# Kernel optimization log

Hardware: AMD Instinct MI355X
Metric: run time of the kernel (lower is better)

## Reference

```python
import jax, jax.numpy as jnp
import numpy as np

EPS_RMS = 1e-6
Q_CLIP_MIN = 1e-5

def setup_inputs() -> dict:
    key = jax.random.key(0)
    k1, k2 = jax.random.split(key)
    x = jax.random.normal(k1, (1, 2048, 4096), dtype=jnp.float32)
    # kaiming_uniform-ish init for weight [in_features, out_features]
    fan_in = 4096
    bound = 1.0 / np.sqrt(fan_in)
    weight = jax.random.uniform(k2, (4096, 4096), dtype=jnp.float32, minval=-bound, maxval=bound)
    rms_weight = jnp.ones((4096,), dtype=jnp.float32)
    return {"x": x, "weight": weight, "rms_weight": rms_weight}

def reference(x, weight, rms_weight):
    # RMSNorm over last dim
    xn = x * jax.lax.rsqrt(jnp.mean(x * x, axis=-1, keepdims=True) + EPS_RMS) * rms_weight
    K = weight.shape[0]
    orig_shape = xn.shape
    x2 = xn.reshape(-1, K)  # [M, K]

    # per-tensor absmax int8 activation quantization
    a_scale = 127.0 / jnp.clip(jnp.max(jnp.abs(x2)), Q_CLIP_MIN)
    A_q = jnp.clip(jnp.round(x2 * a_scale), -128.0, 127.0)

    # absmean ternary weight quantization
    b_scale = 1.0 / jnp.clip(jnp.mean(jnp.abs(weight)), Q_CLIP_MIN)
    B_t = jnp.clip(jnp.round(weight * b_scale), -1.0, 1.0)

    # integer matmul + dequant: (A_q @ B_t) / (a_scale * b_scale)
    out = (A_q @ B_t) / (a_scale * b_scale)  # [M, N]
    return out.reshape(*orig_shape[:-1], weight.shape[1])
```

## Files before the change

### kernel.cpp

```cpp
#include <hip/hip_runtime.h>
#include <cstdint>

#define M_DIM 2048
#define K_DIM 4096
#define N_DIM 4096

#define BM 256
#define BN 128
#define BK 128
#define KT (K_DIM / BK)
#define A_TILE_BYTES (BM * BK)
#define B_TILE_BYTES (BN * BK)
#define TILE_BYTES (A_TILE_BYTES + B_TILE_BYTES)
#define NBUF 3
#define LDS_BYTES (NBUF * TILE_BYTES)

typedef __attribute__((ext_vector_type(4))) int i32x4;

__device__ __forceinline__ void gload_lds16(const void* g, void* l) {
  __builtin_amdgcn_global_load_lds(
      (__attribute__((address_space(1))) void*)(g),
      (__attribute__((address_space(3))) void*)(l), 16, 0, 0);
}

__global__ void fused_reduce_kernel(const float* __restrict__ x,
                                    const float* __restrict__ rw,
                                    const float* __restrict__ w,
                                    float* __restrict__ invrms,
                                    float* __restrict__ rowmax,
                                    double* __restrict__ partials) {
  const int tid = threadIdx.x;
  __shared__ double red[4];
  __shared__ float redf[4];
  __shared__ float sInv;

  if (blockIdx.x < 2048) {
    const int row = blockIdx.x;
    const float4* xr = (const float4*)(x + (size_t)row * K_DIM);
    const float4* wr = (const float4*)rw;
    float4 xv[4];
    double ss = 0.0;
#pragma unroll
    for (int i = 0; i < 4; i++) {
      xv[i] = xr[i * 256 + tid];
      ss += (double)xv[i].x * xv[i].x + (double)xv[i].y * xv[i].y +
            (double)xv[i].z * xv[i].z + (double)xv[i].w * xv[i].w;
    }
    for (int off = 32; off; off >>= 1) ss += __shfl_down(ss, off);
    if ((tid & 63) == 0) red[tid >> 6] = ss;
    __syncthreads();
    if (tid == 0) {
      double t = red[0] + red[1] + red[2] + red[3];
      sInv = (float)(1.0 / sqrt(t * (1.0 / (double)K_DIM) + 1e-6));
    }
    __syncthreads();
    const float inv = sInv;
    if (tid == 0) invrms[row] = inv;

    float amax = 0.f;
#pragma unroll
    for (int i = 0; i < 4; i++) {
      float4 wv = wr[i * 256 + tid];
      amax = fmaxf(amax, fabsf((xv[i].x * inv) * wv.x));
      amax = fmaxf(amax, fabsf((xv[i].y * inv) * wv.y));
      amax = fmaxf(amax, fabsf((xv[i].z * inv) * wv.z));
      amax = fmaxf(amax, fabsf((xv[i].w * inv) * wv.w));
    }
    for (int off = 32; off; off >>= 1) amax = fmaxf(amax, __shfl_down(amax, off));
    if ((tid & 63) == 0) redf[tid >> 6] = amax;
    __syncthreads();
    if (tid == 0)
      rowmax[row] = fmaxf(fmaxf(redf[0], redf[1]), fmaxf(redf[2], redf[3]));
  } else {
    const int bid = blockIdx.x - 2048;
    const float4* w4 = (const float4*)w;
    const size_t base = (size_t)bid * 2048;
    double s = 0.0;
#pragma unroll
    for (int i = 0; i < 8; i++) {
      float4 v = w4[base + i * 256 + tid];
      s += (double)((fabsf(v.x) + fabsf(v.y)) + (fabsf(v.z) + fabsf(v.w)));
    }
    for (int off = 32; off; off >>= 1) s += __shfl_down(s, off);
    if ((tid & 63) == 0) red[tid >> 6] = s;
    __syncthreads();
    if (tid == 0) partials[bid] = red[0] + red[1] + red[2] + red[3];
  }
}

__global__ void scales_kernel(const float* __restrict__ rowmax,
                              const double* __restrict__ partials,
                              float* __restrict__ scales) {
  const int tid = threadIdx.x;
  float m = 0.f;
  double s = 0.0;
#pragma unroll
  for (int i = 0; i < 8; i++) {
    m = fmaxf(m, rowmax[i * 256 + tid]);
    s += partials[i * 256 + tid];
  }
  for (int off = 32; off; off >>= 1) {
    m = fmaxf(m, __shfl_down(m, off));
    s += __shfl_down(s, off);
  }
  __shared__ float redf[4];
  __shared__ double red[4];
  if ((tid & 63) == 0) { redf[tid >> 6] = m; red[tid >> 6] = s; }
  __syncthreads();
  if (tid == 0) {
    float amax = fmaxf(fmaxf(redf[0], redf[1]), fmaxf(redf[2], redf[3]));
    double wsum = red[0] + red[1] + red[2] + red[3];
    float as = 127.0f / fmaxf(amax, 1e-5f);
    float mean_f = (float)(wsum * (1.0 / 16777216.0));
    float bs = 1.0f / fmaxf(mean_f, 1e-5f);
    scales[0] = as;
    scales[1] = bs;
    scales[2] = 1.0f / (as * bs);
  }
}

__global__ void fused_quant_kernel(const float* __restrict__ x,
                                   const float* __restrict__ rw,
                                   const float* __restrict__ invrms,
                                   const float* __restrict__ scales,
                                   const float* __restrict__ w,
                                   char* __restrict__ Aq,
                                   char* __restrict__ Bt) {
  const int tid = threadIdx.x;
  if (blockIdx.x < 2048) {
    const int row = blockIdx.x;
    const float inv = invrms[row];
    const float as = scales[0];
    const float4* xr = (const float4*)(x + (size_t)row * K_DIM);
    const float4* wr = (const float4*)rw;
    union { char c[16]; int4 v; } o;
#pragma unroll
    for (int i = 0; i < 4; i++) {
      float4 xv = xr[tid * 4 + i];
      float4 wv = wr[tid * 4 + i];
      float t0 = (xv.x * inv) * wv.x;
      float t1 = (xv.y * inv) * wv.y;
      float t2 = (xv.z * inv) * wv.z;
      float t3 = (xv.w * inv) * wv.w;
      o.c[i * 4 + 0] = (char)(int)fminf(fmaxf(rintf(t0 * as), -128.f), 127.f);
      o.c[i * 4 + 1] = (char)(int)fminf(fmaxf(rintf(t1 * as), -128.f), 127.f);
      o.c[i * 4 + 2] = (char)(int)fminf(fmaxf(rintf(t2 * as), -128.f), 127.f);
      o.c[i * 4 + 3] = (char)(int)fminf(fmaxf(rintf(t3 * as), -128.f), 127.f);
    }
    *(int4*)(Aq + (size_t)row * K_DIM + tid * 16) = o.v;
  } else {
    __shared__ float lds[64][68];
    const int tile = blockIdx.x - 2048;
    const int n0 = (tile & 63) * 64;
    const int k0 = (tile >> 6) * 64;
    const float bs = scales[1];
#pragma unroll
    for (int i = 0; i < 4; i++) {
      const int id = i * 256 + tid;
      const int r = id >> 4;
      const int c4 = (id & 15) * 4;
      float4 v = *(const float4*)(w + (size_t)(k0 + r) * N_DIM + n0 + c4);
      lds[c4 + 0][r] = fminf(fmaxf(rintf(v.x * bs), -1.f), 1.f);
      lds[c4 + 1][r] = fminf(fmaxf(rintf(v.y * bs), -1.f), 1.f);
      lds[c4 + 2][r] = fminf(fmaxf(rintf(v.z * bs), -1.f), 1.f);
      lds[c4 + 3][r] = fminf(fmaxf(rintf(v.w * bs), -1.f), 1.f);
    }
    __syncthreads();
    const int rn = tid >> 2;
    const int kg = (tid & 3) * 16;
    union { char c[16]; int4 v; } o;
#pragma unroll
    for (int j = 0; j < 16; j++) o.c[j] = (char)(int)lds[rn][kg + j];
    *(int4*)(Bt + (size_t)(n0 + rn) * K_DIM + k0 + kg) = o.v;
  }
}

__global__ void __launch_bounds__(256, 1)
gemm_kernel(const char* __restrict__ Aq, const char* __restrict__ Bt,
            float* __restrict__ out, const float* __restrict__ scales) {
  extern __shared__ char lds[];
  const int tid = threadIdx.x;
  const int lane = tid & 63;
  const int wave = tid >> 6;
  const int wm = wave >> 1;
  const int wn = wave & 1;
  const int brow = blockIdx.y * BM;
  const int bcol = blockIdx.x * BN;

  i32x4 acc[8][4];
#pragma unroll
  for (int m = 0; m < 8; m++)
#pragma unroll
    for (int n = 0; n < 4; n++) acc[m][n] = {0, 0, 0, 0};

  const int sRow8 = lane >> 3;
  const int srcColB = ((lane & 7) ^ sRow8) * 16;

#define STAGE_A(kt, bi, s)                                                        \
  gload_lds16(Aq + (size_t)(brow + (s)*32 + wave * 8 + sRow8) * K_DIM +           \
                  (kt)*BK + srcColB,                                              \
              lds + (bi)*TILE_BYTES + (s)*4096 + wave * 1024 + lane * 16)
#define STAGE_B(kt, bi, s)                                                        \
  gload_lds16(Bt + (size_t)(bcol + (s)*32 + wave * 8 + sRow8) * K_DIM +           \
                  (kt)*BK + srcColB,                                              \
              lds + (bi)*TILE_BYTES + A_TILE_BYTES + (s)*4096 + wave * 1024 +     \
                  lane * 16)

#pragma unroll
  for (int s = 0; s < 8; s++) STAGE_A(0, 0, s);
#pragma unroll
  for (int s = 0; s < 4; s++) STAGE_B(0, 0, s);
#pragma unroll
  for (int s = 0; s < 8; s++) STAGE_A(1, 1, s);
#pragma unroll
  for (int s = 0; s < 4; s++) STAGE_B(1, 1, s);
  asm volatile("s_waitcnt vmcnt(12)" ::: "memory");
  __builtin_amdgcn_s_barrier();

  const int aBase = (wm * 128 + (lane & 15)) * BK;
  const int bBase = (wn * 64 + (lane & 15)) * BK;
  const int swz0 = ((0 + (lane >> 4)) ^ (lane & 7)) * 16;
  const int swz1 = ((4 + (lane >> 4)) ^ (lane & 7)) * 16;

  i32x4 a0[8], a1[8], bb[8];

#pragma unroll
  for (int m = 0; m < 4; m++) {
    a0[m * 2 + 0] = *(const i32x4*)(lds + aBase + m * 2048 + swz0);
    a0[m * 2 + 1] = *(const i32x4*)(lds + aBase + m * 2048 + swz1);
  }
#pragma unroll
  for (int n = 0; n < 4; n++) {
    bb[n * 2 + 0] = *(const i32x4*)(lds + A_TILE_BYTES + bBase + n * 2048 + swz0);
    bb[n * 2 + 1] = *(const i32x4*)(lds + A_TILE_BYTES + bBase + n * 2048 + swz1);
  }

  int bi = 0;
  for (int t = 0; t < KT; ++t) {
    const char* bufA = lds + bi * TILE_BYTES;
    const int si = (bi + 2 >= NBUF) ? bi + 2 - NBUF : bi + 2;
    const bool doStage = (t + 2) < KT;

    __builtin_amdgcn_s_barrier();
    __builtin_amdgcn_sched_barrier(0);

    if (doStage) {
      STAGE_A(t + 2, si, 0); STAGE_A(t + 2, si, 1); STAGE_A(t + 2, si, 2);
      STAGE_A(t + 2, si, 3); STAGE_A(t + 2, si, 4); STAGE_A(t + 2, si, 5);
    }
#pragma unroll
    for (int m = 0; m < 4; m++) {
      a1[m * 2 + 0] = *(const i32x4*)(bufA + aBase + (m + 4) * 2048 + swz0);
      a1[m * 2 + 1] = *(const i32x4*)(bufA + aBase + (m + 4) * 2048 + swz1);
    }
    asm volatile("s_waitcnt lgkmcnt(8)" ::: "memory");
    __builtin_amdgcn_sched_barrier(0);
    __builtin_amdgcn_s_setprio(1);
#pragma unroll
    for (int m = 0; m < 4; m++)
#pragma unroll
      for (int n = 0; n < 4; n++)
#pragma unroll
        for (int ks = 0; ks < 2; ks++)
          acc[m][n] = __builtin_amdgcn_mfma_i32_16x16x64_i8(
              a0[m * 2 + ks], bb[n * 2 + ks], acc[m][n], 0, 0, 0);
    __builtin_amdgcn_s_setprio(0);

    if (doStage) {
      STAGE_A(t + 2, si, 6); STAGE_A(t + 2, si, 7);
      STAGE_B(t + 2, si, 0); STAGE_B(t + 2, si, 1);
      STAGE_B(t + 2, si, 2); STAGE_B(t + 2, si, 3);
    }
    asm volatile("s_waitcnt lgkmcnt(0)" ::: "memory");
    __builtin_amdgcn_sched_barrier(0);
    __builtin_amdgcn_s_setprio(1);
#pragma unroll
    for (int m = 0; m < 4; m++)
#pragma unroll
      for (int n = 0; n < 4; n++)
#pragma unroll
        for (int ks = 0; ks < 2; ks++)
          acc[m + 4][n] = __builtin_amdgcn_mfma_i32_16x16x64_i8(
              a1[m * 2 + ks], bb[n * 2 + ks], acc[m + 4][n], 0, 0, 0);
    __builtin_amdgcn_s_setprio(0);

    if (t + 1 < KT) {
      if (doStage) {
        asm volatile("s_waitcnt vmcnt(12)" ::: "memory");
      } else {
        asm volatile("s_waitcnt vmcnt(0)" ::: "memory");
      }
      __builtin_amdgcn_sched_barrier(0);
      const int ni = (bi + 1 >= NBUF) ? 0 : bi + 1;
      const char* nA = lds + ni * TILE_BYTES;
      const char* nB = nA + A_TILE_BYTES;
#pragma unroll
      for (int m = 0; m < 4; m++) {
        a0[m * 2 + 0] = *(const i32x4*)(nA + aBase + m * 2048 + swz0);
        a0[m * 2 + 1] = *(const i32x4*)(nA + aBase + m * 2048 + swz1);
      }
#pragma unroll
      for (int n = 0; n < 4; n++) {
        bb[n * 2 + 0] = *(const i32x4*)(nB + bBase + n * 2048 + swz0);
        bb[n * 2 + 1] = *(const i32x4*)(nB + bBase + n * 2048 + swz1);
      }
    }
    bi = (bi + 1 >= NBUF) ? 0 : bi + 1;
  }
#undef STAGE_A
#undef STAGE_B

  const float dq = scales[2];
#pragma unroll
  for (int m = 0; m < 8; m++) {
#pragma unroll
    for (int n = 0; n < 4; n++) {
      const int row = wm * 128 + m * 16 + (lane >> 4) * 4;
      const int col = wn * 64 + n * 16 + (lane & 15);
#pragma unroll
      for (int j = 0; j < 4; j++) {
        out[(size_t)(brow + row + j) * N_DIM + bcol + col] = (float)acc[m][n][j] * dq;
      }
    }
  }
}

extern "C" void kernel_launch(void* const* d_in, const int* in_sizes, int n_in,
                              void* d_out, int out_size, void* d_ws, size_t ws_size,
                              hipStream_t stream) {
  const float* x      = (const float*)d_in[0];
  const float* weight = (const float*)d_in[1];
  const float* rms_w  = (const float*)d_in[2];
  float* out = (float*)d_out;

  uint8_t* ws = (uint8_t*)d_ws;
  float* scales    = (float*)(ws + 0);
  float* invrms    = (float*)(ws + 64);
  float* rowmax    = (float*)(ws + 64 + 8192);
  double* partials = (double*)(ws + 64 + 16384);
  char* Aq = (char*)(ws + 65536);
  char* Bt = (char*)(ws + 65536 + (size_t)M_DIM * K_DIM);

  (void)hipFuncSetAttribute((const void*)gemm_kernel,
                            hipFuncAttributeMaxDynamicSharedMemorySize, LDS_BYTES);

  fused_reduce_kernel<<<4096, 256, 0, stream>>>(x, rms_w, weight, invrms, rowmax, partials);
  scales_kernel<<<1, 256, 0, stream>>>(rowmax, partials, scales);
  fused_quant_kernel<<<6144, 256, 0, stream>>>(x, rms_w, invrms, scales, weight, Aq, Bt);
  gemm_kernel<<<dim3(N_DIM / BN, M_DIM / BM), 256, LDS_BYTES, stream>>>(Aq, Bt, out, scales);
}
```

Before: 77.04 us.

## Shrink GEMM tiles to 128x128 with two-wave blocks, double buffering, and block swizzle

The int8 GEMM tile changes from 256x128 with four waves and triple buffering to 128x128 with two waves and double buffering, launched as 512 blocks over a 1D grid. A block-index swizzle groups neighbouring blocks so they share A/B tiles in cache. The goal is more blocks for better CU occupancy and load balance, at the cost of more global traffic per output and a simpler prefetch pipeline with less latency hiding.

New measurement: 80.38 us. +4.3%, slower.

```diff
diff --git a/kernel.cpp b/kernel.cpp
--- a/kernel.cpp
+++ b/kernel.cpp
@@ -5,14 +5,14 @@
 #define K_DIM 4096
 #define N_DIM 4096
 
-#define BM 256
+#define BM 128
 #define BN 128
 #define BK 128
 #define KT (K_DIM / BK)
 #define A_TILE_BYTES (BM * BK)
 #define B_TILE_BYTES (BN * BK)
 #define TILE_BYTES (A_TILE_BYTES + B_TILE_BYTES)
-#define NBUF 3
+#define NBUF 2
 #define LDS_BYTES (NBUF * TILE_BYTES)
 
 typedef __attribute__((ext_vector_type(4))) int i32x4;
@@ -175,17 +175,19 @@
   }
 }
 
-__global__ void __launch_bounds__(256, 1)
+__global__ void __launch_bounds__(128, 1)
 gemm_kernel(const char* __restrict__ Aq, const char* __restrict__ Bt,
             float* __restrict__ out, const float* __restrict__ scales) {
   extern __shared__ char lds[];
   const int tid = threadIdx.x;
   const int lane = tid & 63;
-  const int wave = tid >> 6;
-  const int wm = wave >> 1;
-  const int wn = wave & 1;
-  const int brow = blockIdx.y * BM;
-  const int bcol = blockIdx.x * BN;
+  const int wv = tid >> 6;
+  const int flat = blockIdx.x;
+  const int swzb = (flat & 7) * 64 + (flat >> 3);
+  const int bx = swzb & 31;
+  const int by = swzb >> 5;
+  const int brow = by * BM;
+  const int bcol = bx * BN;
 
   i32x4 acc[8][4];
 #pragma unroll
@@ -197,115 +199,74 @@
   const int srcColB = ((lane & 7) ^ sRow8) * 16;
 
 #define STAGE_A(kt, bi, s)                                                        \
-  gload_lds16(Aq + (size_t)(brow + (s)*32 + wave * 8 + sRow8) * K_DIM +           \
+  gload_lds16(Aq + (size_t)(brow + (s)*16 + wv * 8 + sRow8) * K_DIM +             \
                   (kt)*BK + srcColB,                                              \
-              lds + (bi)*TILE_BYTES + (s)*4096 + wave * 1024 + lane * 16)
+              lds + (bi)*TILE_BYTES + ((s)*16 + wv * 8) * 128 + lane * 16)
 #define STAGE_B(kt, bi, s)                                                        \
-  gload_lds16(Bt + (size_t)(bcol + (s)*32 + wave * 8 + sRow8) * K_DIM +           \
+  gload_lds16(Bt + (size_t)(bcol + (s)*16 + wv * 8 + sRow8) * K_DIM +             \
                   (kt)*BK + srcColB,                                              \
-              lds + (bi)*TILE_BYTES + A_TILE_BYTES + (s)*4096 + wave * 1024 +     \
+              lds + (bi)*TILE_BYTES + A_TILE_BYTES + ((s)*16 + wv * 8) * 128 +    \
                   lane * 16)
 
 #pragma unroll
   for (int s = 0; s < 8; s++) STAGE_A(0, 0, s);
 #pragma unroll
-  for (int s = 0; s < 4; s++) STAGE_B(0, 0, s);
-#pragma unroll
-  for (int s = 0; s < 8; s++) STAGE_A(1, 1, s);
-#pragma unroll
-  for (int s = 0; s < 4; s++) STAGE_B(1, 1, s);
-  asm volatile("s_waitcnt vmcnt(12)" ::: "memory");
-  __builtin_amdgcn_s_barrier();
-
-  const int aBase = (wm * 128 + (lane & 15)) * BK;
-  const int bBase = (wn * 64 + (lane & 15)) * BK;
+  for (int s = 0; s < 8; s++) STAGE_B(0, 0, s);
+
+  const int aBase = (lane & 15) * BK;
+  const int bBase = (wv * 64 + (lane & 15)) * BK;
   const int swz0 = ((0 + (lane >> 4)) ^ (lane & 7)) * 16;
   const int swz1 = ((4 + (lane >> 4)) ^ (lane & 7)) * 16;
 
-  i32x4 a0[8], a1[8], bb[8];
-
-#pragma unroll
-  for (int m = 0; m < 4; m++) {
-    a0[m * 2 + 0] = *(const i32x4*)(lds + aBase + m * 2048 + swz0);
-    a0[m * 2 + 1] = *(const i32x4*)(lds + aBase + m * 2048 + swz1);
-  }
-#pragma unroll
-  for (int n = 0; n < 4; n++) {
-    bb[n * 2 + 0] = *(const i32x4*)(lds + A_TILE_BYTES + bBase + n * 2048 + swz0);
-    bb[n * 2 + 1] = *(const i32x4*)(lds + A_TILE_BYTES + bBase + n * 2048 + swz1);
-  }
-
-  int bi = 0;
   for (int t = 0; t < KT; ++t) {
+    const int bi = t & 1;
     const char* bufA = lds + bi * TILE_BYTES;
-    const int si = (bi + 2 >= NBUF) ? bi + 2 - NBUF : bi + 2;
-    const bool doStage = (t + 2) < KT;
+    const char* bufB = bufA + A_TILE_BYTES;
 
     __builtin_amdgcn_s_barrier();
     __builtin_amdgcn_sched_barrier(0);
-
-    if (doStage) {
-      STAGE_A(t + 2, si, 0); STAGE_A(t + 2, si, 1); STAGE_A(t + 2, si, 2);
-      STAGE_A(t + 2, si, 3); STAGE_A(t + 2, si, 4); STAGE_A(t + 2, si, 5);
-    }
-#pragma unroll
-    for (int m = 0; m < 4; m++) {
-      a1[m * 2 + 0] = *(const i32x4*)(bufA + aBase + (m + 4) * 2048 + swz0);
-      a1[m * 2 + 1] = *(const i32x4*)(bufA + aBase + (m + 4) * 2048 + swz1);
-    }
-    asm volatile("s_waitcnt lgkmcnt(8)" ::: "memory");
+    if (t + 1 < KT) {
+      const int si = (t + 1) & 1;
+#pragma unroll
+      for (int s = 0; s < 8; s++) STAGE_A(t + 1, si, s);
+#pragma unroll
+      for (int s = 0; s < 8; s++) STAGE_B(t + 1, si, s);
+      asm volatile("s_waitcnt vmcnt(16)" ::: "memory");
+    } else {
+      asm volatile("s_waitcnt vmcnt(0)" ::: "memory");
+    }
+    __builtin_amdgcn_sched_barrier(0);
+
+    i32x4 a0[8], a1[8], b0[4], b1[4];
+#pragma unroll
+    for (int m = 0; m < 8; m++) a0[m] = *(const i32x4*)(bufA + aBase + m * 2048 + swz0);
+#pragma unroll
+    for (int n = 0; n < 4; n++) b0[n] = *(const i32x4*)(bufB + bBase + n * 2048 + swz0);
+    __builtin_amdgcn_sched_barrier(0);
+#pragma unroll
+    for (int m = 0; m < 8; m++) a1[m] = *(const i32x4*)(bufA + aBase + m * 2048 + swz1);
+#pragma unroll
+    for (int n = 0; n < 4; n++) b1[n] = *(const i32x4*)(bufB + bBase + n * 2048 + swz1);
+
+    asm volatile("s_waitcnt lgkmcnt(12)" ::: "memory");
     __builtin_amdgcn_sched_barrier(0);
     __builtin_amdgcn_s_setprio(1);
 #pragma unroll
-    for (int m = 0; m < 4; m++)
+    for (int m = 0; m < 8; m++)
 #pragma unroll
       for (int n = 0; n < 4; n++)
-#pragma unroll
-        for (int ks = 0; ks < 2; ks++)
-          acc[m][n] = __builtin_amdgcn_mfma_i32_16x16x64_i8(
-              a0[m * 2 + ks], bb[n * 2 + ks], acc[m][n], 0, 0, 0);
+        acc[m][n] = __builtin_amdgcn_mfma_i32_16x16x64_i8(a0[m], b0[n], acc[m][n], 0, 0, 0);
     __builtin_amdgcn_s_setprio(0);
 
-    if (doStage) {
-      STAGE_A(t + 2, si, 6); STAGE_A(t + 2, si, 7);
-      STAGE_B(t + 2, si, 0); STAGE_B(t + 2, si, 1);
-      STAGE_B(t + 2, si, 2); STAGE_B(t + 2, si, 3);
-    }
     asm volatile("s_waitcnt lgkmcnt(0)" ::: "memory");
     __builtin_amdgcn_sched_barrier(0);
     __builtin_amdgcn_s_setprio(1);
 #pragma unroll
-    for (int m = 0; m < 4; m++)
+    for (int m = 0; m < 8; m++)
 #pragma unroll
       for (int n = 0; n < 4; n++)
-#pragma unroll
-        for (int ks = 0; ks < 2; ks++)
-          acc[m + 4][n] = __builtin_amdgcn_mfma_i32_16x16x64_i8(
-              a1[m * 2 + ks], bb[n * 2 + ks], acc[m + 4][n], 0, 0, 0);
+        acc[m][n] = __builtin_amdgcn_mfma_i32_16x16x64_i8(a1[m], b1[n], acc[m][n], 0, 0, 0);
     __builtin_amdgcn_s_setprio(0);
-
-    if (t + 1 < KT) {
-      if (doStage) {
-        asm volatile("s_waitcnt vmcnt(12)" ::: "memory");
-      } else {
-        asm volatile("s_waitcnt vmcnt(0)" ::: "memory");
-      }
-      __builtin_amdgcn_sched_barrier(0);
-      const int ni = (bi + 1 >= NBUF) ? 0 : bi + 1;
-      const char* nA = lds + ni * TILE_BYTES;
-      const char* nB = nA + A_TILE_BYTES;
-#pragma unroll
-      for (int m = 0; m < 4; m++) {
-        a0[m * 2 + 0] = *(const i32x4*)(nA + aBase + m * 2048 + swz0);
-        a0[m * 2 + 1] = *(const i32x4*)(nA + aBase + m * 2048 + swz1);
-      }
-#pragma unroll
-      for (int n = 0; n < 4; n++) {
-        bb[n * 2 + 0] = *(const i32x4*)(nB + bBase + n * 2048 + swz0);
-        bb[n * 2 + 1] = *(const i32x4*)(nB + bBase + n * 2048 + swz1);
-      }
-    }
-    bi = (bi + 1 >= NBUF) ? 0 : bi + 1;
   }
 #undef STAGE_A
 #undef STAGE_B
@@ -315,8 +276,8 @@
   for (int m = 0; m < 8; m++) {
 #pragma unroll
     for (int n = 0; n < 4; n++) {
-      const int row = wm * 128 + m * 16 + (lane >> 4) * 4;
-      const int col = wn * 64 + n * 16 + (lane & 15);
+      const int row = m * 16 + (lane >> 4) * 4;
+      const int col = wv * 64 + n * 16 + (lane & 15);
 #pragma unroll
       for (int j = 0; j < 4; j++) {
         out[(size_t)(brow + row + j) * N_DIM + bcol + col] = (float)acc[m][n][j] * dq;
@@ -347,5 +308,5 @@
   fused_reduce_kernel<<<4096, 256, 0, stream>>>(x, rms_w, weight, invrms, rowmax, partials);
   scales_kernel<<<1, 256, 0, stream>>>(rowmax, partials, scales);
   fused_quant_kernel<<<6144, 256, 0, stream>>>(x, rms_w, invrms, scales, weight, Aq, Bt);
-  gemm_kernel<<<dim3(N_DIM / BN, M_DIM / BM), 256, LDS_BYTES, stream>>>(Aq, Bt, out, scales);
-}
+  gemm_kernel<<<512, 128, LDS_BYTES, stream>>>(Aq, Bt, out, scales);
+}
```
